# Kernel tuning notes

Hardware: AMD Instinct MI355X
Metric: run time of the kernel (lower is better)

The kernel has to match this reference:

```python
import jax, jax.numpy as jnp
import numpy as np

N, E, F_IN, H, C, G, NCLS = 50000, 400000, 128, 8, 64, 64, 10
NEG_SLOPE = 0.2
EPS = 1e-16


def gat_conv(x, W, att_src, att_dst, bias, src, dst, concat):
    n = x.shape[0]
    h = (x @ W).reshape(n, H, C)                      # [N,H,C]
    a_src = jnp.sum(h * att_src, axis=-1)             # [N,H]
    a_dst = jnp.sum(h * att_dst, axis=-1)             # [N,H]
    alpha = jax.nn.leaky_relu(a_src[src] + a_dst[dst], NEG_SLOPE)  # [E,H]
    # segment softmax over incoming edges of each destination node
    amax = jax.ops.segment_max(alpha, dst, num_segments=n)
    ex = jnp.exp(alpha - amax[dst])
    denom = jax.ops.segment_sum(ex, dst, num_segments=n)
    alpha = ex / (denom[dst] + EPS)
    msg = h[src] * alpha[:, :, None]                  # [E,H,C]
    out = jax.ops.segment_sum(msg, dst, num_segments=n)  # [N,H,C]
    out = out.reshape(n, H * C) if concat else out.mean(axis=1)
    return out + bias


def setup_inputs() -> dict:
    key = jax.random.key(0)
    ks = jax.random.split(key, 20)
    x = jax.random.normal(ks[0], (N, F_IN), dtype=jnp.float32)
    edge_index = jax.random.randint(ks[1], (2, E), 0, N, dtype=jnp.int32)
    batch = jnp.sort(jax.random.randint(ks[2], (N,), 0, G, dtype=jnp.int32))
    def glorot(k, shape):
        fan = sum(shape[-2:]) if len(shape) >= 2 else shape[-1]
        return jax.random.normal(k, shape, dtype=jnp.float32) * jnp.sqrt(2.0 / fan)
    return {
        "x": x, "edge_index": edge_index, "batch": batch,
        "W1": glorot(ks[3], (F_IN, H * C)),
        "a1s": glorot(ks[4], (H, C)), "a1d": glorot(ks[5], (H, C)),
        "b1": jnp.zeros((H * C,), jnp.float32),
        "W2": glorot(ks[6], (H * C, H * C)),
        "a2s": glorot(ks[7], (H, C)), "a2d": glorot(ks[8], (H, C)),
        "b2": jnp.zeros((H * C,), jnp.float32),
        "W3": glorot(ks[9], (H * C, H * C)),
        "a3s": glorot(ks[10], (H, C)), "a3d": glorot(ks[11], (H, C)),
        "b3": jnp.zeros((C,), jnp.float32),
        "fcw": glorot(ks[12], (C, NCLS)),
        "fcb": jnp.zeros((NCLS,), jnp.float32),
    }


def reference(x, edge_index, batch, W1, a1s, a1d, b1, W2, a2s, a2d, b2,
              W3, a3s, a3d, b3, fcw, fcb):
    n = x.shape[0]
    # PyG GATConv default add_self_loops=True
    loops = jnp.arange(n, dtype=edge_index.dtype)
    src = jnp.concatenate([edge_index[0], loops])
    dst = jnp.concatenate([edge_index[1], loops])

    h = jax.nn.relu(gat_conv(x, W1, a1s, a1d, b1, src, dst, True))
    h = jax.nn.relu(gat_conv(h, W2, a2s, a2d, b2, src, dst, True))
    h = jax.nn.relu(gat_conv(h, W3, a3s, a3d, b3, src, dst, False))  # [N,C]

    # global mean pool over graphs
    sums = jax.ops.segment_sum(h, batch, num_segments=G)
    cnts = jax.ops.segment_sum(jnp.ones((n, 1), h.dtype), batch, num_segments=G)
    pooled = sums / jnp.maximum(cnts, 1.0)            # [G,C]

    return jax.nn.log_softmax(pooled @ fcw + fcb, axis=-1)
```

## Files before the change

kernel.cpp:

```cpp
#include <hip/hip_runtime.h>
#include <hip/hip_bf16.h>

#define HH 8
#define CC 64
#define HC 512
#define GG 64
#define NCLS 10
#define F_IN 128
#define NEG_SLOPE 0.2f
#define EPS_ 1e-16f
#define MAXD 32

typedef float f32x4 __attribute__((ext_vector_type(4)));
typedef __bf16 bf16x8 __attribute__((ext_vector_type(8)));

__device__ __forceinline__ unsigned short f2bf(float f) {
    unsigned u = __builtin_bit_cast(unsigned, f);
    u += 0x7fffu + ((u >> 16) & 1u);
    return (unsigned short)(u >> 16);
}
__device__ __forceinline__ float bflo(unsigned u) {
    return __builtin_bit_cast(float, u << 16);
}
__device__ __forceinline__ float bfhi(unsigned u) {
    return __builtin_bit_cast(float, u & 0xffff0000u);
}
__device__ __forceinline__ unsigned char f2fp8(float f) {
    unsigned pk = __builtin_amdgcn_cvt_pk_fp8_f32(f, f, 0u, false);
    return (unsigned char)(pk & 0xffu);
}
template <int SEL>
__device__ __forceinline__ float fp82f(unsigned w) {
    return __builtin_amdgcn_cvt_f32_fp8(w, SEL);
}
#define ACC_FP8(hv, w)                                           \
    acc[0] += (w) * fp82f<0>(hv.x); acc[1] += (w) * fp82f<1>(hv.x); \
    acc[2] += (w) * fp82f<2>(hv.x); acc[3] += (w) * fp82f<3>(hv.x); \
    acc[4] += (w) * fp82f<0>(hv.y); acc[5] += (w) * fp82f<1>(hv.y); \
    acc[6] += (w) * fp82f<2>(hv.y); acc[7] += (w) * fp82f<3>(hv.y);

__device__ __forceinline__ void gload16(const unsigned short* g, unsigned short* l) {
    __builtin_amdgcn_global_load_lds(
        (const __attribute__((address_space(1))) unsigned int*)g,
        (__attribute__((address_space(3))) unsigned int*)l,
        16, 0, 0);
}

__global__ void hist_kernel(const int* __restrict__ ei, int* __restrict__ counts,
                            int E_, int EP_) {
    int e = blockIdx.x * 256 + threadIdx.x;
    if (e >= EP_) return;
    int d = (e < E_) ? ei[E_ + e] : (e - E_);
    atomicAdd(&counts[d], 1);
}

__global__ void scan1(const int* __restrict__ counts, int* __restrict__ partial,
                      int* __restrict__ bsum, int n) {
    __shared__ int buf[256];
    int idx = blockIdx.x * 256 + threadIdx.x;
    int v = (idx < n) ? counts[idx] : 0;
    buf[threadIdx.x] = v;
    __syncthreads();
    for (int off = 1; off < 256; off <<= 1) {
        int t = (threadIdx.x >= off) ? buf[threadIdx.x - off] : 0;
        __syncthreads();
        buf[threadIdx.x] += t;
        __syncthreads();
    }
    if (idx < n) partial[idx] = buf[threadIdx.x];
    if (threadIdx.x == 255) bsum[blockIdx.x] = buf[255];
}

__global__ void scan2(int* __restrict__ bsum, int nb) {
    __shared__ int buf[1024];
    int t = threadIdx.x;
    buf[t] = (t < nb) ? bsum[t] : 0;
    __syncthreads();
    for (int off = 1; off < 1024; off <<= 1) {
        int v = (t >= off) ? buf[t - off] : 0;
        __syncthreads();
        buf[t] += v;
        __syncthreads();
    }
    if (t < nb) bsum[t] = buf[t];
}

__global__ void scan3(const int* __restrict__ partial, const int* __restrict__ bsum,
                      int* __restrict__ row_start, int* __restrict__ counts, int n) {
    int idx = blockIdx.x * 256 + threadIdx.x;
    if (idx >= n) return;
    int add = (blockIdx.x > 0) ? bsum[blockIdx.x - 1] : 0;
    row_start[idx + 1] = partial[idx] + add;
    counts[idx] = 0;
    if (idx == 0) row_start[0] = 0;
}

__global__ void scatter_kernel(const int* __restrict__ ei, const int* __restrict__ row_start,
                               int* __restrict__ cursor, int* __restrict__ src_sorted,
                               int E_, int EP_) {
    int e = blockIdx.x * 256 + threadIdx.x;
    if (e >= EP_) return;
    int s, d;
    if (e < E_) { s = ei[e]; d = ei[E_ + e]; }
    else        { s = e - E_; d = e - E_; }
    int pos = row_start[d] + atomicAdd(&cursor[d], 1);
    src_sorted[pos] = s;
}

__global__ void conv_bf16(const float* __restrict__ in, unsigned short* __restrict__ out,
                          int n4) {
    int i = blockIdx.x * 256 + threadIdx.x;
    if (i >= n4) return;
    float4 v = reinterpret_cast<const float4*>(in)[i];
    reinterpret_cast<ushort4*>(out)[i] =
        make_ushort4(f2bf(v.x), f2bf(v.y), f2bf(v.z), f2bf(v.w));
}

__global__ void transpose_w(const float* __restrict__ W, unsigned short* __restrict__ WT,
                            int K, int Nc) {
    __shared__ float t[32][33];
    int bx = blockIdx.x * 32;
    int by = blockIdx.y * 32;
    int x = threadIdx.x, y = threadIdx.y;
    for (int i = y; i < 32; i += 8)
        t[i][x] = W[(size_t)(by + i) * Nc + bx + x];
    __syncthreads();
    for (int i = y; i < 32; i += 8)
        WT[(size_t)(bx + i) * K + by + x] = f2bf(t[x][i]);
}

__global__ __launch_bounds__(256) void gemm_attn(const unsigned short* __restrict__ A,
                                                 const unsigned short* __restrict__ BT,
                                                 unsigned char* __restrict__ C,
                                                 const float* __restrict__ asw,
                                                 const float* __restrict__ adw,
                                                 float* __restrict__ a_src,
                                                 float* __restrict__ a_dst,
                                                 int M, int K) {
    __shared__ __align__(16) unsigned short As[128 * 64];
    __shared__ __align__(16) unsigned short Bs[128 * 64];

    const int nwg = gridDim.x;
    const int f = blockIdx.x;
    const int q = nwg >> 3, r = nwg & 7;
    const int xcd = f & 7, rank = f >> 3;
    const int swz = (xcd < r ? xcd * (q + 1) : r * (q + 1) + (xcd - r) * q) + rank;
    const int bcol = (swz & 3) * 128;
    const int brow = (swz >> 2) * 128;

    const int tid = threadIdx.x;
    const int lane = tid & 63;
    const int wave = tid >> 6;
    const int wr = wave >> 1, wc = wave & 1;

    f32x4 acc[4][4];
#pragma unroll
    for (int i = 0; i < 4; ++i)
#pragma unroll
        for (int j = 0; j < 4; ++j) acc[i][j] = (f32x4)0.f;

    const int lrow = lane >> 3;
    const int lcolsw = (((lane & 7) ^ lrow)) * 8;
    const int arow0 = brow + wave * 32 + lrow;
    const int brow0 = bcol + wave * 32 + lrow;

    const int kb = (lane >> 4) * 8;
    const int rowa = wr * 64 + (lane & 15);
    const int rowb = wc * 64 + (lane & 15);
    const int rxor = lane & 7;

    for (int k0 = 0; k0 < K; k0 += 64) {
#pragma unroll
        for (int it = 0; it < 4; ++it) {
            const int c = wave * 4 + it;
            int ar = arow0 + it * 8;
            if (ar >= M) ar = M - 1;
            gload16(A + (size_t)ar * K + k0 + lcolsw, &As[c * 512]);
            int br = brow0 + it * 8;
            gload16(BT + (size_t)br * K + k0 + lcolsw, &Bs[c * 512]);
        }
        __syncthreads();
#pragma unroll
        for (int kk = 0; kk < 64; kk += 32) {
            const int chunk = (kk + kb) >> 3;
            const int koff = (chunk ^ rxor) * 8;
            bf16x8 a[4], b[4];
#pragma unroll
            for (int m = 0; m < 4; ++m)
                a[m] = *(const bf16x8*)&As[(rowa + m * 16) * 64 + koff];
#pragma unroll
            for (int nn = 0; nn < 4; ++nn)
                b[nn] = *(const bf16x8*)&Bs[(rowb + nn * 16) * 64 + koff];
#pragma unroll
            for (int m = 0; m < 4; ++m)
#pragma unroll
                for (int nn = 0; nn < 4; ++nn)
                    acc[m][nn] = __builtin_amdgcn_mfma_f32_16x16x32_bf16(
                        a[m], b[nn], acc[m][nn], 0, 0, 0);
        }
        __syncthreads();
    }

    const int r0 = brow + wr * 64 + (lane >> 4) * 4;
    const int c0 = bcol + wc * 64 + (lane & 15);

#pragma unroll
    for (int m = 0; m < 4; ++m)
#pragma unroll
        for (int j = 0; j < 4; ++j) {
            int rr = r0 + m * 16 + j;
            if (rr < M) {
#pragma unroll
                for (int nn = 0; nn < 4; ++nn)
                    C[(size_t)rr * HC + c0 + nn * 16] = f2fp8(acc[m][nn][j]);
            }
        }

    const int head = (bcol + wc * 64) >> 6;
    float asv[4], adv[4];
#pragma unroll
    for (int nn = 0; nn < 4; ++nn) {
        int c = c0 + nn * 16;
        asv[nn] = asw[c];
        adv[nn] = adw[c];
    }
    float psrc[4][4], pdst[4][4];
#pragma unroll
    for (int m = 0; m < 4; ++m)
#pragma unroll
        for (int j = 0; j < 4; ++j) {
            float ps = 0.f, pd = 0.f;
#pragma unroll
            for (int nn = 0; nn < 4; ++nn) {
                float hv = acc[m][nn][j];
                ps += hv * asv[nn];
                pd += hv * adv[nn];
            }
            psrc[m][j] = ps;
            pdst[m][j] = pd;
        }
#pragma unroll
    for (int m = 0; m < 4; ++m)
#pragma unroll
        for (int j = 0; j < 4; ++j) {
#pragma unroll
            for (int mask = 1; mask < 16; mask <<= 1) {
                psrc[m][j] += __shfl_xor(psrc[m][j], mask);
                pdst[m][j] += __shfl_xor(pdst[m][j], mask);
            }
        }
    if ((lane & 15) == 0) {
#pragma unroll
        for (int m = 0; m < 4; ++m)
#pragma unroll
            for (int j = 0; j < 4; ++j) {
                int rr = r0 + m * 16 + j;
                if (rr < M) {
                    a_src[rr * 8 + head] = psrc[m][j];
                    a_dst[rr * 8 + head] = pdst[m][j];
                }
            }
    }
}

template <int MODE>
__global__ __launch_bounds__(256) void agg_kernel(const unsigned char* __restrict__ h,
                                                  const float* __restrict__ a_src,
                                                  const float* __restrict__ a_dst,
                                                  const float* __restrict__ bias,
                                                  const int* __restrict__ row_start,
                                                  const int* __restrict__ src_sorted,
                                                  void* __restrict__ outv, int n) {
    __shared__ float alds[4][MAXD][8];
    __shared__ int   slds[4][MAXD];
    int ws = threadIdx.x >> 6;
    int d = blockIdx.x * 4 + ws;
    int lane = threadIdx.x & 63;
    if (d >= n) return;
    int base = row_start[d];
    int end = row_start[d + 1];
    int deg = end - base;
    int head = lane & 7;
    int eslot = lane >> 3;
    float adh = a_dst[d * 8 + head];

    float mx = -1e30f;
    for (int idx = eslot; idx < deg; idx += 8) {
        int s = src_sorted[base + idx];
        float al = a_src[s * 8 + head] + adh;
        al = (al > 0.f) ? al : NEG_SLOPE * al;
        if (idx < MAXD) {
            alds[ws][idx][head] = al;
            if (head == 0) slds[ws][idx] = s;
        }
        mx = fmaxf(mx, al);
    }
    mx = fmaxf(mx, __shfl_xor(mx, 8));
    mx = fmaxf(mx, __shfl_xor(mx, 16));
    mx = fmaxf(mx, __shfl_xor(mx, 32));

    float sm = 0.f;
    for (int idx = eslot; idx < deg; idx += 8) {
        float e;
        if (idx < MAXD) {
            float al = alds[ws][idx][head];
            e = __expf(al - mx);
            alds[ws][idx][head] = e;
        } else {
            int s = src_sorted[base + idx];
            float al = a_src[s * 8 + head] + adh;
            al = (al > 0.f) ? al : NEG_SLOPE * al;
            e = __expf(al - mx);
        }
        sm += e;
    }
    sm += __shfl_xor(sm, 8);
    sm += __shfl_xor(sm, 16);
    sm += __shfl_xor(sm, 32);
    float inv = 1.0f / (sm + EPS_);

    asm volatile("s_waitcnt lgkmcnt(0)" ::: "memory");
    __builtin_amdgcn_wave_barrier();

    int hd2 = lane >> 3;
    float mx2 = __shfl(mx, hd2);
    float inv2 = __shfl(inv, hd2);
    float adh2 = a_dst[d * 8 + hd2];
    const unsigned char* hl = h + lane * 8;

    float acc[8] = {};
    int mdeg = (deg < MAXD) ? deg : MAXD;
    for (int i = 0; i < mdeg; i += 4) {
        int i0 = i;
        int i1 = (i + 1 < mdeg) ? i + 1 : mdeg - 1;
        int i2 = (i + 2 < mdeg) ? i + 2 : mdeg - 1;
        int i3 = (i + 3 < mdeg) ? i + 3 : mdeg - 1;
        int s0 = slds[ws][i0], s1 = slds[ws][i1];
        int s2 = slds[ws][i2], s3 = slds[ws][i3];
        uint2 h0 = *reinterpret_cast<const uint2*>(hl + (size_t)s0 * HC);
        uint2 h1 = *reinterpret_cast<const uint2*>(hl + (size_t)s1 * HC);
        uint2 h2 = *reinterpret_cast<const uint2*>(hl + (size_t)s2 * HC);
        uint2 h3 = *reinterpret_cast<const uint2*>(hl + (size_t)s3 * HC);
        float w0 = alds[ws][i0][hd2] * inv2;
        float w1 = (i + 1 < mdeg) ? alds[ws][i1][hd2] * inv2 : 0.f;
        float w2 = (i + 2 < mdeg) ? alds[ws][i2][hd2] * inv2 : 0.f;
        float w3 = (i + 3 < mdeg) ? alds[ws][i3][hd2] * inv2 : 0.f;
        ACC_FP8(h0, w0)
        ACC_FP8(h1, w1)
        ACC_FP8(h2, w2)
        ACC_FP8(h3, w3)
    }
    for (int i = base + MAXD; i < end; ++i) {
        int s = src_sorted[i];
        float al = a_src[s * 8 + hd2] + adh2;
        al = (al > 0.f) ? al : NEG_SLOPE * al;
        float w = __expf(al - mx2) * inv2;
        uint2 hv = *reinterpret_cast<const uint2*>(hl + (size_t)s * HC);
        ACC_FP8(hv, w)
    }

    if (MODE == 0) {
        float4 b0 = *reinterpret_cast<const float4*>(bias + lane * 8);
        float4 b1 = *reinterpret_cast<const float4*>(bias + lane * 8 + 4);
        float v[8];
        v[0] = fmaxf(acc[0] + b0.x, 0.f); v[1] = fmaxf(acc[1] + b0.y, 0.f);
        v[2] = fmaxf(acc[2] + b0.z, 0.f); v[3] = fmaxf(acc[3] + b0.w, 0.f);
        v[4] = fmaxf(acc[4] + b1.x, 0.f); v[5] = fmaxf(acc[5] + b1.y, 0.f);
        v[6] = fmaxf(acc[6] + b1.z, 0.f); v[7] = fmaxf(acc[7] + b1.w, 0.f);
        uint4 o;
        o.x = (unsigned)f2bf(v[0]) | ((unsigned)f2bf(v[1]) << 16);
        o.y = (unsigned)f2bf(v[2]) | ((unsigned)f2bf(v[3]) << 16);
        o.z = (unsigned)f2bf(v[4]) | ((unsigned)f2bf(v[5]) << 16);
        o.w = (unsigned)f2bf(v[6]) | ((unsigned)f2bf(v[7]) << 16);
        *reinterpret_cast<uint4*>((unsigned short*)outv + (size_t)d * HC + lane * 8) = o;
    } else {
#pragma unroll
        for (int j = 0; j < 8; ++j) {
            acc[j] += __shfl_xor(acc[j], 8);
            acc[j] += __shfl_xor(acc[j], 16);
            acc[j] += __shfl_xor(acc[j], 32);
        }
        if (lane < 8) {
            float* op = (float*)outv + (size_t)d * 64 + lane * 8;
            float4 o0, o1;
            o0.x = fmaxf(acc[0] * 0.125f + bias[lane * 8 + 0], 0.f);
            o0.y = fmaxf(acc[1] * 0.125f + bias[lane * 8 + 1], 0.f);
            o0.z = fmaxf(acc[2] * 0.125f + bias[lane * 8 + 2], 0.f);
            o0.w = fmaxf(acc[3] * 0.125f + bias[lane * 8 + 3], 0.f);
            o1.x = fmaxf(acc[4] * 0.125f + bias[lane * 8 + 4], 0.f);
            o1.y = fmaxf(acc[5] * 0.125f + bias[lane * 8 + 5], 0.f);
            o1.z = fmaxf(acc[6] * 0.125f + bias[lane * 8 + 6], 0.f);
            o1.w = fmaxf(acc[7] * 0.125f + bias[lane * 8 + 7], 0.f);
            *reinterpret_cast<float4*>(op) = o0;
            *reinterpret_cast<float4*>(op + 4) = o1;
        }
    }
}

__global__ __launch_bounds__(256) void pool_classify(const float* __restrict__ h3,
                                                     const int* __restrict__ batch,
                                                     const float* __restrict__ fcw,
                                                     const float* __restrict__ fcb,
                                                     float* __restrict__ out, int n) {
    int g = blockIdx.x;
    __shared__ int s_lo, s_hi;
    if (threadIdx.x == 0) {
        int lo = 0, hi = n;
        while (lo < hi) { int mid = (lo + hi) >> 1; if (batch[mid] < g) lo = mid + 1; else hi = mid; }
        s_lo = lo;
        int lo2 = lo, hi2 = n;
        while (lo2 < hi2) { int mid = (lo2 + hi2) >> 1; if (batch[mid] < g + 1) lo2 = mid + 1; else hi2 = mid; }
        s_hi = lo2;
    }
    __syncthreads();
    int lo = s_lo, hi = s_hi;
    int lane = threadIdx.x & 63;
    int slot = threadIdx.x >> 6;
    float acc = 0.f;
    for (int i = lo + slot; i < hi; i += 4)
        acc += h3[(size_t)i * 64 + lane];
    __shared__ float red[4][64];
    red[slot][lane] = acc;
    __syncthreads();
    if (slot == 0) {
        float v = red[0][lane] + red[1][lane] + red[2][lane] + red[3][lane];
        float c = (float)(hi - lo);
        c = fmaxf(c, 1.0f);
        float p = v / c;
        float logit[NCLS];
#pragma unroll
        for (int j = 0; j < NCLS; ++j) {
            float t = p * fcw[lane * NCLS + j];
#pragma unroll
            for (int off = 1; off < 64; off <<= 1) t += __shfl_xor(t, off);
            logit[j] = t + fcb[j];
        }
        float m = logit[0];
#pragma unroll
        for (int j = 1; j < NCLS; ++j) m = fmaxf(m, logit[j]);
        float s = 0.f;
#pragma unroll
        for (int j = 0; j < NCLS; ++j) s += expf(logit[j] - m);
        float lse = logf(s);
        if (lane < NCLS) {
            float vv = logit[0];
#pragma unroll
            for (int j = 1; j < NCLS; ++j)
                if (lane == j) vv = logit[j];
            out[g * NCLS + lane] = vv - m - lse;
        }
    }
}

extern "C" void kernel_launch(void* const* d_in, const int* in_sizes, int n_in,
                              void* d_out, int out_size, void* d_ws, size_t ws_size,
                              hipStream_t stream) {
    const float* x    = (const float*)d_in[0];
    const int*   ei   = (const int*)d_in[1];
    const int*   batch = (const int*)d_in[2];
    const float* W1  = (const float*)d_in[3];
    const float* a1s = (const float*)d_in[4];
    const float* a1d = (const float*)d_in[5];
    const float* b1  = (const float*)d_in[6];
    const float* W2  = (const float*)d_in[7];
    const float* a2s = (const float*)d_in[8];
    const float* a2d = (const float*)d_in[9];
    const float* b2  = (const float*)d_in[10];
    const float* W3  = (const float*)d_in[11];
    const float* a3s = (const float*)d_in[12];
    const float* a3d = (const float*)d_in[13];
    const float* b3  = (const float*)d_in[14];
    const float* fcw = (const float*)d_in[15];
    const float* fcb = (const float*)d_in[16];

    const int n  = in_sizes[0] / F_IN;
    const int E_ = in_sizes[1] / 2;
    const int EP = E_ + n;

    char* p = (char*)d_ws;
    unsigned short* xb   = (unsigned short*)p; p += (size_t)n * F_IN * 2;
    unsigned short* w1t  = (unsigned short*)p; p += (size_t)HC * F_IN * 2;
    unsigned short* w2t  = (unsigned short*)p; p += (size_t)HC * HC * 2;
    unsigned short* w3t  = (unsigned short*)p; p += (size_t)HC * HC * 2;
    unsigned char*  hbuf = (unsigned char*)p;  p += (size_t)n * HC;
    unsigned short* buf2 = (unsigned short*)p; p += (size_t)n * HC * 2;
    float* asrc   = (float*)p; p += (size_t)n * 8 * 4;
    float* adst   = (float*)p; p += (size_t)n * 8 * 4;
    float* h3     = (float*)p; p += (size_t)n * 64 * 4;
    int* counts   = (int*)p;   p += (size_t)n * 4;
    int* row_start= (int*)p;   p += (size_t)(n + 1) * 4;
    int* src_sorted=(int*)p;   p += (size_t)EP * 4;
    int* partial  = (int*)p;   p += (size_t)n * 4;
    int* bsum     = (int*)p;   p += 1024 * 4;

    const int edge_blocks = (EP + 255) / 256;
    const int node_blocks = (n + 3) / 4;
    const int scan_blocks = (n + 255) / 256;

    hipMemsetAsync(counts, 0, (size_t)n * sizeof(int), stream);
    hist_kernel<<<edge_blocks, 256, 0, stream>>>(ei, counts, E_, EP);
    scan1<<<scan_blocks, 256, 0, stream>>>(counts, partial, bsum, n);
    scan2<<<1, 1024, 0, stream>>>(bsum, scan_blocks);
    scan3<<<scan_blocks, 256, 0, stream>>>(partial, bsum, row_start, counts, n);
    scatter_kernel<<<edge_blocks, 256, 0, stream>>>(ei, row_start, counts, src_sorted, E_, EP);

    conv_bf16<<<((n * F_IN / 4) + 255) / 256, 256, 0, stream>>>(x, xb, n * F_IN / 4);
    transpose_w<<<dim3(HC / 32, F_IN / 32), dim3(32, 8), 0, stream>>>(W1, w1t, F_IN, HC);
    transpose_w<<<dim3(HC / 32, HC / 32), dim3(32, 8), 0, stream>>>(W2, w2t, HC, HC);
    transpose_w<<<dim3(HC / 32, HC / 32), dim3(32, 8), 0, stream>>>(W3, w3t, HC, HC);

    const int nby = (n + 127) / 128;
    const int nwg = 4 * nby;

    gemm_attn<<<nwg, 256, 0, stream>>>(xb, w1t, hbuf, a1s, a1d, asrc, adst, n, F_IN);
    agg_kernel<0><<<node_blocks, 256, 0, stream>>>(hbuf, asrc, adst, b1, row_start, src_sorted, buf2, n);

    gemm_attn<<<nwg, 256, 0, stream>>>(buf2, w2t, hbuf, a2s, a2d, asrc, adst, n, HC);
    agg_kernel<0><<<node_blocks, 256, 0, stream>>>(hbuf, asrc, adst, b2, row_start, src_sorted, buf2, n);

    gemm_attn<<<nwg, 256, 0, stream>>>(buf2, w3t, hbuf, a3s, a3d, asrc, adst, n, HC);
    agg_kernel<1><<<node_blocks, 256, 0, stream>>>(hbuf, asrc, adst, b3, row_start, src_sorted, h3, n);

    pool_classify<<<GG, 256, 0, stream>>>(h3, batch, fcw, fcb, (float*)d_out, n);
}
```

Baseline: 413.2 us.

## Fold attention vectors into weights and compute scores via extra MFMA columns

Precomputes W·att_src and W·att_dst per head as a 16-column bf16 matrix, then computes a_src/a_dst inside the GEMM as extra MFMA tiles on column-block 0 only. This replaces the per-tile epilogue dot products and 16-step shuffle reductions done by every workgroup. In exchange it adds three small prep kernels, extra LDS loads and MFMAs on one quarter of the workgroups (load imbalance), and slightly different rounding because the folded weights are stored in bf16.

```diff
diff --git a/kernel.cpp b/kernel.cpp
--- a/kernel.cpp
+++ b/kernel.cpp
@@ -129,16 +129,42 @@
         WT[(size_t)(bx + i) * K + by + x] = f2bf(t[x][i]);
 }
 
+__global__ void make_wsd(const float* __restrict__ W, const float* __restrict__ as_,
+                         const float* __restrict__ ad_, unsigned short* __restrict__ BX,
+                         int K) {
+    int k = blockIdx.x;
+    int lane = threadIdx.x & 63;
+    int head = lane >> 3;
+    int coff = (lane & 7) * 8;
+    const float* wr = W + (size_t)k * HC + head * 64 + coff;
+    const float* asp = as_ + head * 64 + coff;
+    const float* adp = ad_ + head * 64 + coff;
+    float ps = 0.f, pd = 0.f;
+#pragma unroll
+    for (int i = 0; i < 8; ++i) {
+        float wv = wr[i];
+        ps += wv * asp[i];
+        pd += wv * adp[i];
+    }
+    ps += __shfl_xor(ps, 1); pd += __shfl_xor(pd, 1);
+    ps += __shfl_xor(ps, 2); pd += __shfl_xor(pd, 2);
+    ps += __shfl_xor(ps, 4); pd += __shfl_xor(pd, 4);
+    if ((lane & 7) == 0) {
+        BX[(size_t)head * K + k] = f2bf(ps);
+        BX[(size_t)(8 + head) * K + k] = f2bf(pd);
+    }
+}
+
 __global__ __launch_bounds__(256) void gemm_attn(const unsigned short* __restrict__ A,
                                                  const unsigned short* __restrict__ BT,
+                                                 const unsigned short* __restrict__ BX,
                                                  unsigned char* __restrict__ C,
-                                                 const float* __restrict__ asw,
-                                                 const float* __restrict__ adw,
                                                  float* __restrict__ a_src,
                                                  float* __restrict__ a_dst,
                                                  int M, int K) {
     __shared__ __align__(16) unsigned short As[128 * 64];
     __shared__ __align__(16) unsigned short Bs[128 * 64];
+    __shared__ __align__(16) unsigned short Bxs[16 * 64];
 
     const int nwg = gridDim.x;
     const int f = blockIdx.x;
@@ -152,12 +178,16 @@
     const int lane = tid & 63;
     const int wave = tid >> 6;
     const int wr = wave >> 1, wc = wave & 1;
+    const bool do_x = (wc == 0) && (bcol == 0);
 
     f32x4 acc[4][4];
 #pragma unroll
     for (int i = 0; i < 4; ++i)
 #pragma unroll
         for (int j = 0; j < 4; ++j) acc[i][j] = (f32x4)0.f;
+    f32x4 accx[4];
+#pragma unroll
+    for (int i = 0; i < 4; ++i) accx[i] = (f32x4)0.f;
 
     const int lrow = lane >> 3;
     const int lcolsw = (((lane & 7) ^ lrow)) * 8;
@@ -179,6 +209,8 @@
             int br = brow0 + it * 8;
             gload16(BT + (size_t)br * K + k0 + lcolsw, &Bs[c * 512]);
         }
+        if (bcol == 0 && wave < 2)
+            gload16(BX + (size_t)(wave * 8 + lrow) * K + k0 + lcolsw, &Bxs[wave * 512]);
         __syncthreads();
 #pragma unroll
         for (int kk = 0; kk < 64; kk += 32) {
@@ -197,6 +229,13 @@
                 for (int nn = 0; nn < 4; ++nn)
                     acc[m][nn] = __builtin_amdgcn_mfma_f32_16x16x32_bf16(
                         a[m], b[nn], acc[m][nn], 0, 0, 0);
+            if (do_x) {
+                bf16x8 bx = *(const bf16x8*)&Bxs[(lane & 15) * 64 + koff];
+#pragma unroll
+                for (int m = 0; m < 4; ++m)
+                    accx[m] = __builtin_amdgcn_mfma_f32_16x16x32_bf16(
+                        a[m], bx, accx[m], 0, 0, 0);
+            }
         }
         __syncthreads();
     }
@@ -216,49 +255,16 @@
             }
         }
 
-    const int head = (bcol + wc * 64) >> 6;
-    float asv[4], adv[4];
-#pragma unroll
-    for (int nn = 0; nn < 4; ++nn) {
-        int c = c0 + nn * 16;
-        asv[nn] = asw[c];
-        adv[nn] = adw[c];
-    }
-    float psrc[4][4], pdst[4][4];
-#pragma unroll
-    for (int m = 0; m < 4; ++m)
-#pragma unroll
-        for (int j = 0; j < 4; ++j) {
-            float ps = 0.f, pd = 0.f;
-#pragma unroll
-            for (int nn = 0; nn < 4; ++nn) {
-                float hv = acc[m][nn][j];
-                ps += hv * asv[nn];
-                pd += hv * adv[nn];
-            }
-            psrc[m][j] = ps;
-            pdst[m][j] = pd;
-        }
-#pragma unroll
-    for (int m = 0; m < 4; ++m)
-#pragma unroll
-        for (int j = 0; j < 4; ++j) {
-#pragma unroll
-            for (int mask = 1; mask < 16; mask <<= 1) {
-                psrc[m][j] += __shfl_xor(psrc[m][j], mask);
-                pdst[m][j] += __shfl_xor(pdst[m][j], mask);
-            }
-        }
-    if ((lane & 15) == 0) {
+    if (do_x) {
+        const int col16 = lane & 15;
+        float* dst = (col16 < 8) ? a_src : a_dst;
+        const int head = col16 & 7;
 #pragma unroll
         for (int m = 0; m < 4; ++m)
 #pragma unroll
             for (int j = 0; j < 4; ++j) {
                 int rr = r0 + m * 16 + j;
-                if (rr < M) {
-                    a_src[rr * 8 + head] = psrc[m][j];
-                    a_dst[rr * 8 + head] = pdst[m][j];
-                }
+                if (rr < M) dst[rr * 8 + head] = accx[m][j];
             }
     }
 }
@@ -482,6 +488,9 @@
     unsigned short* w1t  = (unsigned short*)p; p += (size_t)HC * F_IN * 2;
     unsigned short* w2t  = (unsigned short*)p; p += (size_t)HC * HC * 2;
     unsigned short* w3t  = (unsigned short*)p; p += (size_t)HC * HC * 2;
+    unsigned short* bx1  = (unsigned short*)p; p += (size_t)16 * F_IN * 2;
+    unsigned short* bx2  = (unsigned short*)p; p += (size_t)16 * HC * 2;
+    unsigned short* bx3  = (unsigned short*)p; p += (size_t)16 * HC * 2;
     unsigned char*  hbuf = (unsigned char*)p;  p += (size_t)n * HC;
     unsigned short* buf2 = (unsigned short*)p; p += (size_t)n * HC * 2;
     float* asrc   = (float*)p; p += (size_t)n * 8 * 4;
@@ -508,17 +517,20 @@
     transpose_w<<<dim3(HC / 32, F_IN / 32), dim3(32, 8), 0, stream>>>(W1, w1t, F_IN, HC);
     transpose_w<<<dim3(HC / 32, HC / 32), dim3(32, 8), 0, stream>>>(W2, w2t, HC, HC);
     transpose_w<<<dim3(HC / 32, HC / 32), dim3(32, 8), 0, stream>>>(W3, w3t, HC, HC);
+    make_wsd<<<F_IN, 64, 0, stream>>>(W1, a1s, a1d, bx1, F_IN);
+    make_wsd<<<HC, 64, 0, stream>>>(W2, a2s, a2d, bx2, HC);
+    make_wsd<<<HC, 64, 0, stream>>>(W3, a3s, a3d, bx3, HC);
 
     const int nby = (n + 127) / 128;
     const int nwg = 4 * nby;
 
-    gemm_attn<<<nwg, 256, 0, stream>>>(xb, w1t, hbuf, a1s, a1d, asrc, adst, n, F_IN);
+    gemm_attn<<<nwg, 256, 0, stream>>>(xb, w1t, bx1, hbuf, asrc, adst, n, F_IN);
     agg_kernel<0><<<node_blocks, 256, 0, stream>>>(hbuf, asrc, adst, b1, row_start, src_sorted, buf2, n);
 
-    gemm_attn<<<nwg, 256, 0, stream>>>(buf2, w2t, hbuf, a2s, a2d, asrc, adst, n, HC);
+    gemm_attn<<<nwg, 256, 0, stream>>>(buf2, w2t, bx2, hbuf, asrc, adst, n, HC);
     agg_kernel<0><<<node_blocks, 256, 0, stream>>>(hbuf, asrc, adst, b2, row_start, src_sorted, buf2, n);
 
-    gemm_attn<<<nwg, 256, 0, stream>>>(buf2, w3t, hbuf, a3s, a3d, asrc, adst, n, HC);
+    gemm_attn<<<nwg, 256, 0, stream>>>(buf2, w3t, bx3, hbuf, asrc, adst, n, HC);
     agg_kernel<1><<<node_blocks, 256, 0, stream>>>(hbuf, asrc, adst, b3, row_start, src_sorted, h3, n);
 
     pool_classify<<<GG, 256, 0, stream>>>(h3, batch, fcw, fcb, (float*)d_out, n);
```

After: 389.4 us. 5.8% less time.
